# Kernel tuning notes

Hardware: AMD Instinct MI355X
Metric: run time of the kernel (lower is better)

## Reference

```python
import jax, jax.numpy as jnp
import numpy as np

QUERY_DIM = 512
CAAN_DIM = 512
HID = 30

def setup_inputs() -> dict:
    key = jax.random.key(0)
    ks = jax.random.split(key, 9)
    def lin(kk, out_d, in_d):
        lim = 1.0 / np.sqrt(in_d)
        return jax.random.uniform(kk, (out_d, in_d), jnp.float32, -lim, lim)
    R = jax.random.normal(ks[0], (8, 2048, QUERY_DIM), jnp.float32)
    return {
        "R": R,
        "Wq": lin(ks[1], CAAN_DIM, QUERY_DIM), "bq": jnp.zeros((CAAN_DIM,), jnp.float32),
        "Wk": lin(ks[2], CAAN_DIM, QUERY_DIM), "bk": jnp.zeros((CAAN_DIM,), jnp.float32),
        "Wv": lin(ks[3], CAAN_DIM, QUERY_DIM), "bv": jnp.zeros((CAAN_DIM,), jnp.float32),
        "W1": lin(ks[4], HID, CAAN_DIM), "b1": jax.random.uniform(ks[5], (HID,), jnp.float32, -1/np.sqrt(CAAN_DIM), 1/np.sqrt(CAAN_DIM)),
        "W2": lin(ks[6], 1, HID), "b2": jax.random.uniform(ks[7], (1,), jnp.float32, -1/np.sqrt(HID), 1/np.sqrt(HID)),
    }

def reference(R, Wq, bq, Wk, bk, Wv, bv, W1, b1, W2, b2):
    # Projections: [b, n, d]
    Q = jnp.einsum('bnq,dq->bnd', R, Wq) + bq
    K = jnp.einsum('bnq,dq->bnd', R, Wk) + bk
    V = jnp.einsum('bnq,dq->bnd', R, Wv) + bv
    dk = K.shape[-1]
    # Full score matrix, naive exp-normalize (no max subtraction) as in original
    gamma = jnp.einsum('bnd,bmd->bnm', Q, K) / jnp.sqrt(jnp.float32(dk))
    e = jnp.exp(gamma)
    saat = e / jnp.sum(e, axis=2, keepdims=True)  # [b, n, n]
    a = jnp.einsum('bnm,bmd->bnd', saat, V)       # [b, n, d]
    # fc head: CAAN_dim -> 30 -> 1, squeeze last dim
    h = jnp.einsum('bnd,hd->bnh', a, W1) + b1
    winner_score = (jnp.einsum('bnh,oh->bno', h, W2) + b2)[..., 0]
    return winner_score
```

## Files before the change

### kernel.cpp

```cpp
#include <hip/hip_runtime.h>
#include <math.h>

#define BATCH 8
#define SEQ 2048
#define DIM 512
#define MTOT (BATCH*SEQ)
#define HID 30

typedef short bf16x8 __attribute__((ext_vector_type(8)));
typedef float f32x4 __attribute__((ext_vector_type(4)));

__device__ __forceinline__ unsigned short f2bf(float f) {
  unsigned int u = __float_as_uint(f);
  unsigned int r = (u + 0x7FFFu + ((u >> 16) & 1u)) >> 16;
  return (unsigned short)r;
}

__device__ __forceinline__ void gload_lds16(const void* g, void* l) {
  __builtin_amdgcn_global_load_lds((const __attribute__((address_space(1))) void*)g,
                                   (__attribute__((address_space(3))) void*)l, 16, 0, 0);
}

__device__ __forceinline__ void gemm256_core(const unsigned short* __restrict__ gA,
                                             const unsigned short* __restrict__ gB,
                                             char* smem, f32x4 (&acc)[8][4]) {
  const int t = threadIdx.x;
  const int lane = t & 63;
  const int w = t >> 6;
  const int wr = w >> 2, wc = w & 3;
  const int lr = lane & 15, kc = lane >> 4;
  const int srow = t >> 3;
  const int ss = (t & 7) ^ (srow & 7);
  const unsigned short* gsrc = (ss < 4 ? gA : gB) + (size_t)srow * DIM + (ss & 3) * 8;
  const uint32_t dbase = (uint32_t)(t & 448) * 16;

  auto stage = [&](int buf, int kt) {
#pragma unroll
    for (int q = 0; q < 4; ++q)
      gload_lds16(gsrc + (size_t)(q * 64) * DIM + kt * 32,
                  smem + buf * 32768 + q * 8192 + dbase);
  };

  stage(0, 0); stage(1, 1); stage(2, 2);
  asm volatile("s_waitcnt vmcnt(8)" ::: "memory");
  __builtin_amdgcn_s_barrier();
  asm volatile("" ::: "memory");

#pragma unroll
  for (int kt = 0; kt < 16; ++kt) {
    stage((kt + 3) & 3, (kt + 3 < 16) ? (kt + 3) : 15);
    const char* Ab = smem + (kt & 3) * 32768;
    bf16x8 bfr[4], af[4];
#pragma unroll
    for (int j = 0; j < 4; ++j) {
      int r = wc * 64 + j * 16 + lr;
      bfr[j] = *(const bf16x8*)(Ab + r * 128 + (((4 + kc) ^ (r & 7)) << 4));
    }
#pragma unroll
    for (int i = 0; i < 4; ++i) {
      int r = wr * 128 + i * 16 + lr;
      af[i] = *(const bf16x8*)(Ab + r * 128 + ((kc ^ (r & 7)) << 4));
    }
    __builtin_amdgcn_s_setprio(1);
#pragma unroll
    for (int i = 0; i < 4; ++i)
#pragma unroll
      for (int j = 0; j < 4; ++j)
        acc[i][j] = __builtin_amdgcn_mfma_f32_16x16x32_bf16(af[i], bfr[j], acc[i][j], 0, 0, 0);
    __builtin_amdgcn_s_setprio(0);
#pragma unroll
    for (int i = 0; i < 4; ++i) {
      int r = wr * 128 + (i + 4) * 16 + lr;
      af[i] = *(const bf16x8*)(Ab + r * 128 + ((kc ^ (r & 7)) << 4));
    }
    __builtin_amdgcn_s_setprio(1);
#pragma unroll
    for (int i = 0; i < 4; ++i)
#pragma unroll
      for (int j = 0; j < 4; ++j)
        acc[i + 4][j] = __builtin_amdgcn_mfma_f32_16x16x32_bf16(af[i], bfr[j], acc[i + 4][j], 0, 0, 0);
    __builtin_amdgcn_s_setprio(0);
    asm volatile("s_waitcnt vmcnt(8)" ::: "memory");
    __builtin_amdgcn_s_barrier();
    asm volatile("" ::: "memory");
  }
}

__global__ __launch_bounds__(256) void k_weights(
    const float* __restrict__ Wq, const float* __restrict__ Wk, const float* __restrict__ Wv,
    const float* __restrict__ bq, const float* __restrict__ bv,
    const float* __restrict__ W1, const float* __restrict__ b1,
    const float* __restrict__ W2, const float* __restrict__ b2,
    unsigned short* __restrict__ Gt, float* __restrict__ u,
    float* __restrict__ wv2, float* __restrict__ consts) {
  __shared__ __align__(16) float As[16][68];
  __shared__ __align__(16) float Bs[16][68];
  __shared__ float vecs[512];
  __shared__ float red2[16][17];
  const int bid = blockIdx.x;
  const int t = threadIdx.x;

  if (bid < 64) {
    int tm = t & 15, tn = t >> 4;
    int q1b = (bid & 7) * 64, q2b = (bid >> 3) * 64;
    int lk = t >> 4, lc = (t & 15) * 4;
    float acc[4][4] = {};
    float4 ra = *(const float4*)&Wq[(size_t)lk * DIM + q1b + lc];
    float4 rb = *(const float4*)&Wk[(size_t)lk * DIM + q2b + lc];
    for (int kb = 0; kb < DIM; kb += 16) {
      *(float4*)&As[lk][lc] = ra;
      *(float4*)&Bs[lk][lc] = rb;
      __syncthreads();
      if (kb + 16 < DIM) {
        ra = *(const float4*)&Wq[(size_t)(kb + 16 + lk) * DIM + q1b + lc];
        rb = *(const float4*)&Wk[(size_t)(kb + 16 + lk) * DIM + q2b + lc];
      }
#pragma unroll
      for (int k = 0; k < 16; ++k) {
        float4 av = *(float4*)&As[k][tm * 4];
        float4 bv4 = *(float4*)&Bs[k][tn * 4];
        float a[4] = {av.x, av.y, av.z, av.w};
        float b[4] = {bv4.x, bv4.y, bv4.z, bv4.w};
#pragma unroll
        for (int i = 0; i < 4; ++i)
#pragma unroll
          for (int j = 0; j < 4; ++j) acc[i][j] = fmaf(a[i], b[j], acc[i][j]);
      }
      __syncthreads();
    }
#pragma unroll
    for (int i = 0; i < 4; ++i)
#pragma unroll
      for (int j = 0; j < 4; ++j)
        Gt[(size_t)(q2b + tn * 4 + j) * DIM + (q1b + tm * 4 + i)] = f2bf(acc[i][j]);
    return;
  }

  if (bid < 128) {
    bool isU = bid < 96;
    int qb = (bid - (isU ? 64 : 96)) * 16;
    if (isU) {
      vecs[t] = bq[t];
      vecs[t + 256] = bq[t + 256];
    } else {
      for (int d = t; d < DIM; d += 256) {
        float s = 0.f;
        for (int j = 0; j < HID; ++j) s = fmaf(W2[j], W1[(size_t)j * DIM + d], s);
        vecs[d] = s;
      }
    }
    __syncthreads();
    const float* M = isU ? Wk : Wv;
    int ql = t & 15, ds = t >> 4;
    float s = 0.f;
#pragma unroll 8
    for (int i = 0; i < 32; ++i) {
      int d = ds * 32 + i;
      s = fmaf(vecs[d], M[(size_t)d * DIM + qb + ql], s);
    }
    red2[ds][ql] = s;
    __syncthreads();
    if (t < 16) {
      float r = 0.f;
#pragma unroll
      for (int k = 0; k < 16; ++k) r += red2[k][t];
      (isU ? u : wv2)[qb + t] = r;
    }
    return;
  }

  {
    for (int d = t; d < DIM; d += 256) {
      float s = 0.f;
      for (int j = 0; j < HID; ++j) s = fmaf(W2[j], W1[(size_t)j * DIM + d], s);
      vecs[d] = s;
    }
    __syncthreads();
    float* red = (float*)red2;
    red[t] = bv[t] * vecs[t] + bv[t + 256] * vecs[t + 256];
    __syncthreads();
    for (int o = 128; o > 0; o >>= 1) {
      if (t < o) red[t] += red[t + o];
      __syncthreads();
    }
    if (t == 0) {
      consts[0] = red[0];
      float s = b2[0];
      for (int j = 0; j < HID; ++j) s = fmaf(W2[j], b1[j], s);
      consts[1] = s;
    }
  }
}

__global__ __launch_bounds__(256) void k_conv(const float* __restrict__ R,
                                              const float* __restrict__ wv2,
                                              const float* __restrict__ consts,
                                              unsigned short* __restrict__ Rb16,
                                              float* __restrict__ vw) {
  int wave = threadIdx.x >> 6, lane = threadIdx.x & 63;
  size_t n = (size_t)blockIdx.x * 4 + wave;
  const float* p = &R[n * DIM + lane * 8];
  float4 r0 = *(const float4*)p;
  float4 r1 = *(const float4*)(p + 4);
  ushort4 lo, hi;
  lo.x = f2bf(r0.x); lo.y = f2bf(r0.y); lo.z = f2bf(r0.z); lo.w = f2bf(r0.w);
  hi.x = f2bf(r1.x); hi.y = f2bf(r1.y); hi.z = f2bf(r1.z); hi.w = f2bf(r1.w);
  *(ushort4*)&Rb16[n * DIM + lane * 8] = lo;
  *(ushort4*)&Rb16[n * DIM + lane * 8 + 4] = hi;
  float4 v0 = *(const float4*)&wv2[lane * 8];
  float4 v1 = *(const float4*)&wv2[lane * 8 + 4];
  float sv = r0.x * v0.x + r0.y * v0.y + r0.z * v0.z + r0.w * v0.w +
             r1.x * v1.x + r1.y * v1.y + r1.z * v1.z + r1.w * v1.w;
#pragma unroll
  for (int o = 32; o > 0; o >>= 1) sv += __shfl_xor(sv, o);
  if (lane == 0) vw[n] = sv + consts[0];
}

__global__ __launch_bounds__(512, 2) void k_projT(const unsigned short* __restrict__ Rb16,
                                                  const unsigned short* __restrict__ Gt,
                                                  const float* __restrict__ u,
                                                  unsigned short* __restrict__ Tb16) {
  __shared__ __align__(16) char smem[131072];
  __shared__ float u_lds[256];
  int t = threadIdx.x;
  size_t rowb = (size_t)blockIdx.x * 256;
  int colb = blockIdx.y * 256;
  if (t < 256) u_lds[t] = u[colb + t];
  f32x4 acc[8][4] = {};
  gemm256_core(Rb16 + rowb * DIM, Gt + (size_t)colb * DIM, smem, acc);
  int lane = t & 63, w = t >> 6, wr = w >> 2, wc = w & 3;
  int lr = lane & 15, kq = lane >> 4;
#pragma unroll
  for (int i = 0; i < 8; ++i)
#pragma unroll
    for (int j = 0; j < 4; ++j)
#pragma unroll
      for (int r = 0; r < 4; ++r) {
        int row = wr * 128 + i * 16 + kq * 4 + r;
        int col = wc * 64 + j * 16 + lr;
        Tb16[(rowb + row) * DIM + colb + col] = f2bf(acc[i][j][r] + u_lds[col]);
      }
}

__global__ __launch_bounds__(512, 2) void k_qk(const unsigned short* __restrict__ Tb16,
                                               const unsigned short* __restrict__ Rb16,
                                               const float* __restrict__ vw,
                                               float* __restrict__ part_s1,
                                               float* __restrict__ part_den) {
  __shared__ __align__(16) char smem[131072];
  __shared__ float vw_lds[256];
  __shared__ float red_s1[4][256], red_den[4][256];
  int t = threadIdx.x;
  int orig = blockIdx.x;
  int wgid = (orig & 7) * 64 + (orig >> 3);
  int b = wgid >> 6;
  int nb = ((wgid >> 3) & 7) * 256;
  int mb = (wgid & 7) * 256;
  if (t < 256) vw_lds[t] = vw[b * SEQ + mb + t];
  f32x4 acc[8][4] = {};
  gemm256_core(Tb16 + ((size_t)b * SEQ + nb) * DIM,
               Rb16 + ((size_t)b * SEQ + mb) * DIM, smem, acc);
  int lane = t & 63, w = t >> 6, wr = w >> 2, wc = w & 3;
  int lr = lane & 15, kq = lane >> 4;
  const float rs = 0.044194173824159216f;
  float vwl[4];
#pragma unroll
  for (int j = 0; j < 4; ++j) vwl[j] = vw_lds[wc * 64 + j * 16 + lr];
#pragma unroll
  for (int i = 0; i < 8; ++i) {
#pragma unroll
    for (int r = 0; r < 4; ++r) {
      float sa = 0.f, sd = 0.f;
#pragma unroll
      for (int j = 0; j < 4; ++j) {
        float e = __expf(acc[i][j][r] * rs);
        sa = fmaf(e, vwl[j], sa);
        sd += e;
      }
#pragma unroll
      for (int m = 1; m < 16; m <<= 1) { sa += __shfl_xor(sa, m); sd += __shfl_xor(sd, m); }
      if (lr == 0) {
        int rl = wr * 128 + i * 16 + kq * 4 + r;
        red_s1[wc][rl] = sa;
        red_den[wc][rl] = sd;
      }
    }
  }
  __syncthreads();
  if (t < 256) {
    size_t o = ((size_t)b * 8 + (mb >> 8)) * SEQ + nb + t;
    part_s1[o] = red_s1[0][t] + red_s1[1][t] + red_s1[2][t] + red_s1[3][t];
    part_den[o] = red_den[0][t] + red_den[1][t] + red_den[2][t] + red_den[3][t];
  }
}

__global__ void k_final(const float* __restrict__ part_s1, const float* __restrict__ part_den,
                        const float* __restrict__ consts, float* __restrict__ out) {
  int n = blockIdx.x * 256 + threadIdx.x;
  int b = n >> 11, nn = n & 2047;
  float s1 = 0.f, dn = 0.f;
#pragma unroll
  for (int i = 0; i < 8; ++i) {
    size_t o = ((size_t)b * 8 + i) * SEQ + nn;
    s1 += part_s1[o];
    dn += part_den[o];
  }
  out[n] = s1 / dn + consts[1];
}

extern "C" void kernel_launch(void* const* d_in, const int* in_sizes, int n_in,
                              void* d_out, int out_size, void* d_ws, size_t ws_size,
                              hipStream_t stream) {
  const float* R  = (const float*)d_in[0];
  const float* Wq = (const float*)d_in[1];
  const float* bq = (const float*)d_in[2];
  const float* Wk = (const float*)d_in[3];
  const float* bk = (const float*)d_in[4];
  const float* Wv = (const float*)d_in[5];
  const float* bv = (const float*)d_in[6];
  const float* W1 = (const float*)d_in[7];
  const float* b1 = (const float*)d_in[8];
  const float* W2 = (const float*)d_in[9];
  const float* b2 = (const float*)d_in[10];
  (void)bk;
  float* out = (float*)d_out;

  char* p = (char*)d_ws;
  unsigned short* Rb16 = (unsigned short*)p; p += (size_t)MTOT * DIM * 2;
  unsigned short* Tb16 = (unsigned short*)p; p += (size_t)MTOT * DIM * 2;
  unsigned short* Gt   = (unsigned short*)p; p += (size_t)DIM * DIM * 2;
  float* part_s1  = (float*)p; p += (size_t)BATCH * 8 * SEQ * 4;
  float* part_den = (float*)p; p += (size_t)BATCH * 8 * SEQ * 4;
  float* u      = (float*)p; p += DIM * 4;
  float* wv2    = (float*)p; p += DIM * 4;
  float* vw     = (float*)p; p += MTOT * 4;
  float* consts = (float*)p; p += 16;

  hipLaunchKernelGGL(k_weights, dim3(129), dim3(256), 0, stream,
                     Wq, Wk, Wv, bq, bv, W1, b1, W2, b2, Gt, u, wv2, consts);
  hipLaunchKernelGGL(k_conv, dim3(MTOT / 4), dim3(256), 0, stream, R, wv2, consts, Rb16, vw);
  hipLaunchKernelGGL(k_projT, dim3(MTOT / 256, DIM / 256), dim3(512), 0, stream,
                     Rb16, Gt, u, Tb16);
  hipLaunchKernelGGL(k_qk, dim3(512), dim3(512), 0, stream, Tb16, Rb16, vw, part_s1, part_den);
  hipLaunchKernelGGL(k_final, dim3(MTOT / 256), dim3(256), 0, stream,
                     part_s1, part_den, consts, out);
}
```

Before: 101.2 us.

## Restructure GEMM pipeline to process two k-tiles per barrier

Changes the 4-buffer LDS pipeline from prefetching three tiles ahead with one barrier per k-tile to staging two tiles per step and computing two k-tiles between barriers, waiting on vmcnt(0). A-fragment loads are also interleaved in pairs with MFMAs. The aim is to halve the number of barriers and shrink the live register footprint, at the cost of a shallower prefetch distance and a full drain of outstanding loads each step.

```diff
diff --git a/kernel.cpp b/kernel.cpp
--- a/kernel.cpp
+++ b/kernel.cpp
@@ -41,46 +41,42 @@
                   smem + buf * 32768 + q * 8192 + dbase);
   };
 
-  stage(0, 0); stage(1, 1); stage(2, 2);
-  asm volatile("s_waitcnt vmcnt(8)" ::: "memory");
+  stage(0, 0); stage(1, 1);
+  asm volatile("s_waitcnt vmcnt(0)" ::: "memory");
   __builtin_amdgcn_s_barrier();
   asm volatile("" ::: "memory");
 
 #pragma unroll
-  for (int kt = 0; kt < 16; ++kt) {
-    stage((kt + 3) & 3, (kt + 3 < 16) ? (kt + 3) : 15);
-    const char* Ab = smem + (kt & 3) * 32768;
-    bf16x8 bfr[4], af[4];
-#pragma unroll
-    for (int j = 0; j < 4; ++j) {
-      int r = wc * 64 + j * 16 + lr;
-      bfr[j] = *(const bf16x8*)(Ab + r * 128 + (((4 + kc) ^ (r & 7)) << 4));
-    }
-#pragma unroll
-    for (int i = 0; i < 4; ++i) {
-      int r = wr * 128 + i * 16 + lr;
-      af[i] = *(const bf16x8*)(Ab + r * 128 + ((kc ^ (r & 7)) << 4));
-    }
-    __builtin_amdgcn_s_setprio(1);
-#pragma unroll
-    for (int i = 0; i < 4; ++i)
-#pragma unroll
-      for (int j = 0; j < 4; ++j)
-        acc[i][j] = __builtin_amdgcn_mfma_f32_16x16x32_bf16(af[i], bfr[j], acc[i][j], 0, 0, 0);
-    __builtin_amdgcn_s_setprio(0);
-#pragma unroll
-    for (int i = 0; i < 4; ++i) {
-      int r = wr * 128 + (i + 4) * 16 + lr;
-      af[i] = *(const bf16x8*)(Ab + r * 128 + ((kc ^ (r & 7)) << 4));
-    }
-    __builtin_amdgcn_s_setprio(1);
-#pragma unroll
-    for (int i = 0; i < 4; ++i)
-#pragma unroll
-      for (int j = 0; j < 4; ++j)
-        acc[i + 4][j] = __builtin_amdgcn_mfma_f32_16x16x32_bf16(af[i], bfr[j], acc[i + 4][j], 0, 0, 0);
-    __builtin_amdgcn_s_setprio(0);
-    asm volatile("s_waitcnt vmcnt(8)" ::: "memory");
+  for (int s = 0; s < 8; ++s) {
+    const int t2 = 2 * s + 2, t3 = 2 * s + 3;
+    stage(t2 & 3, (t2 < 16) ? t2 : 15);
+    stage(t3 & 3, (t3 < 16) ? t3 : 15);
+#pragma unroll
+    for (int h = 0; h < 2; ++h) {
+      const int kt = 2 * s + h;
+      const char* Ab = smem + (kt & 3) * 32768;
+      bf16x8 bfr[4];
+#pragma unroll
+      for (int j = 0; j < 4; ++j) {
+        int r = wc * 64 + j * 16 + lr;
+        bfr[j] = *(const bf16x8*)(Ab + r * 128 + (((4 + kc) ^ (r & 7)) << 4));
+      }
+#pragma unroll
+      for (int p = 0; p < 4; ++p) {
+        int r0 = wr * 128 + (2 * p) * 16 + lr;
+        int r1 = wr * 128 + (2 * p + 1) * 16 + lr;
+        bf16x8 a0 = *(const bf16x8*)(Ab + r0 * 128 + ((kc ^ (r0 & 7)) << 4));
+        bf16x8 a1 = *(const bf16x8*)(Ab + r1 * 128 + ((kc ^ (r1 & 7)) << 4));
+        __builtin_amdgcn_s_setprio(1);
+#pragma unroll
+        for (int j = 0; j < 4; ++j) {
+          acc[2 * p][j] = __builtin_amdgcn_mfma_f32_16x16x32_bf16(a0, bfr[j], acc[2 * p][j], 0, 0, 0);
+          acc[2 * p + 1][j] = __builtin_amdgcn_mfma_f32_16x16x32_bf16(a1, bfr[j], acc[2 * p + 1][j], 0, 0, 0);
+        }
+        __builtin_amdgcn_s_setprio(0);
+      }
+    }
+    asm volatile("s_waitcnt vmcnt(0)" ::: "memory");
     __builtin_amdgcn_s_barrier();
     asm volatile("" ::: "memory");
   }
```

After: 106.0 us. 4.7% more time.

## Switch GEMM core to triple-buffered LDS with split interleaved prefetch

Applied to the files above, without the earlier changes.

Changes the shared GEMM mainloop from a 4-slot LDS ring with a 3-stage prefetch to a 3-slot ring with a 2-stage prefetch. Each stage's global-to-LDS loads are split into two halves issued between the MFMA phases, with sched_barriers and extra s_barriers fencing them. This cuts LDS use from 128KB to 96KB per block, which could help occupancy and leaves room for the other shared buffers, and it spreads memory issue across the compute. The cost is shallower latency hiding and two extra workgroup barriers per k-step.

```diff
diff --git a/kernel.cpp b/kernel.cpp
--- a/kernel.cpp
+++ b/kernel.cpp
@@ -29,27 +29,28 @@
   const int w = t >> 6;
   const int wr = w >> 2, wc = w & 3;
   const int lr = lane & 15, kc = lane >> 4;
-  const int srow = t >> 3;
-  const int ss = (t & 7) ^ (srow & 7);
-  const unsigned short* gsrc = (ss < 4 ? gA : gB) + (size_t)srow * DIM + (ss & 3) * 8;
+  const int ss = (t & 7) ^ ((t >> 3) & 7);
+  const unsigned short* gsrc = (ss < 4 ? gA : gB) + (size_t)(t >> 3) * DIM + (ss & 3) * 8;
   const uint32_t dbase = (uint32_t)(t & 448) * 16;
 
-  auto stage = [&](int buf, int kt) {
-#pragma unroll
-    for (int q = 0; q < 4; ++q)
+  auto stage2 = [&](int slot, int kt, int qq) {
+#pragma unroll
+    for (int q = qq; q < qq + 2; ++q)
       gload_lds16(gsrc + (size_t)(q * 64) * DIM + kt * 32,
-                  smem + buf * 32768 + q * 8192 + dbase);
+                  smem + slot * 32768 + q * 8192 + dbase);
   };
 
-  stage(0, 0); stage(1, 1); stage(2, 2);
-  asm volatile("s_waitcnt vmcnt(8)" ::: "memory");
+  stage2(0, 0, 0); stage2(0, 0, 2);
+  stage2(1, 1, 0); stage2(1, 1, 2);
+  asm volatile("s_waitcnt vmcnt(4)" ::: "memory");
   __builtin_amdgcn_s_barrier();
   asm volatile("" ::: "memory");
 
 #pragma unroll
   for (int kt = 0; kt < 16; ++kt) {
-    stage((kt + 3) & 3, (kt + 3 < 16) ? (kt + 3) : 15);
-    const char* Ab = smem + (kt & 3) * 32768;
+    const char* Ab = smem + (kt % 3) * 32768;
+    const int fslot = (kt + 2) % 3;
+    const int src = (kt + 2 < 16) ? (kt + 2) : 15;
     bf16x8 bfr[4], af[4];
 #pragma unroll
     for (int j = 0; j < 4; ++j) {
@@ -61,6 +62,11 @@
       int r = wr * 128 + i * 16 + lr;
       af[i] = *(const bf16x8*)(Ab + r * 128 + ((kc ^ (r & 7)) << 4));
     }
+    __builtin_amdgcn_sched_barrier(0);
+    stage2(fslot, src, 0);
+    __builtin_amdgcn_s_barrier();
+    asm volatile("s_waitcnt lgkmcnt(0)" ::: "memory");
+    __builtin_amdgcn_sched_barrier(0);
     __builtin_amdgcn_s_setprio(1);
 #pragma unroll
     for (int i = 0; i < 4; ++i)
@@ -68,11 +74,18 @@
       for (int j = 0; j < 4; ++j)
         acc[i][j] = __builtin_amdgcn_mfma_f32_16x16x32_bf16(af[i], bfr[j], acc[i][j], 0, 0, 0);
     __builtin_amdgcn_s_setprio(0);
+    __builtin_amdgcn_sched_barrier(0);
+    __builtin_amdgcn_s_barrier();
 #pragma unroll
     for (int i = 0; i < 4; ++i) {
       int r = wr * 128 + (i + 4) * 16 + lr;
       af[i] = *(const bf16x8*)(Ab + r * 128 + ((kc ^ (r & 7)) << 4));
     }
+    __builtin_amdgcn_sched_barrier(0);
+    stage2(fslot, src, 2);
+    __builtin_amdgcn_s_barrier();
+    asm volatile("s_waitcnt lgkmcnt(0)" ::: "memory");
+    __builtin_amdgcn_sched_barrier(0);
     __builtin_amdgcn_s_setprio(1);
 #pragma unroll
     for (int i = 0; i < 4; ++i)
@@ -80,7 +93,8 @@
       for (int j = 0; j < 4; ++j)
         acc[i + 4][j] = __builtin_amdgcn_mfma_f32_16x16x32_bf16(af[i], bfr[j], acc[i + 4][j], 0, 0, 0);
     __builtin_amdgcn_s_setprio(0);
-    asm volatile("s_waitcnt vmcnt(8)" ::: "memory");
+    __builtin_amdgcn_sched_barrier(0);
+    asm volatile("s_waitcnt vmcnt(4)" ::: "memory");
     __builtin_amdgcn_s_barrier();
     asm volatile("" ::: "memory");
   }
@@ -220,7 +234,7 @@
                                                   const unsigned short* __restrict__ Gt,
                                                   const float* __restrict__ u,
                                                   unsigned short* __restrict__ Tb16) {
-  __shared__ __align__(16) char smem[131072];
+  __shared__ __align__(16) char smem[98304];
   __shared__ float u_lds[256];
   int t = threadIdx.x;
   size_t rowb = (size_t)blockIdx.x * 256;
@@ -247,7 +261,7 @@
                                                const float* __restrict__ vw,
                                                float* __restrict__ part_s1,
                                                float* __restrict__ part_den) {
-  __shared__ __align__(16) char smem[131072];
+  __shared__ __align__(16) char smem[98304];
   __shared__ float vw_lds[256];
   __shared__ float red_s1[4][256], red_den[4][256];
   int t = threadIdx.x;
```

Result: faster. 98.29 us (-2.9%).
